# Kernel tuning notes

Measured on AMD Instinct MI355X. Metric: run time of the kernel, lower is better.

The kernel has to match this reference:

```python
import jax, jax.numpy as jnp
import numpy as np

MAX_VAL = 10000.0
KS = (1, 5, 10, 20, 50)
B, V, L = 256, 128000, 200


def setup_inputs() -> dict:
    key = jax.random.key(0)
    k1, k2, k3 = jax.random.split(key, 3)
    scores = jax.random.normal(k1, (B, V), dtype=jnp.float32)
    labels = jax.random.randint(k2, (B,), 0, V, dtype=jnp.int64)
    seqs = jax.random.randint(k3, (B, L), 0, V, dtype=jnp.int64)
    return {"scores": scores, "labels": labels, "seqs": seqs}


def reference(scores, labels, seqs):
    b = scores.shape[0]
    rows = jnp.arange(b)
    # gather predicted score for the true label BEFORE masking (torch order)
    predicts = scores[rows, labels]  # [B]
    # scatter -MAX_VAL at history items (masked scatter)
    masked = scores.at[rows[:, None], seqs].set(-MAX_VAL)  # [B, V]
    valid_length = (masked > -MAX_VAL).sum(-1).astype(jnp.float32)  # [B]
    rank = (predicts[:, None] < masked).sum(-1).astype(jnp.float32)  # [B]
    res = []
    for k in KS:
        indicator = (rank < k).astype(jnp.float32)
        res.append((indicator / jnp.log2(rank + 2.0)).mean())  # NDCG@k
        res.append(indicator.mean())  # Recall@k
    res.append((1.0 / (rank + 1.0)).mean())  # MRR
    res.append((1.0 - rank / valid_length).mean())  # AUC-like
    res.append(jnp.float32(0.0))
    return jnp.stack(res)
```

## Files before the change

### kernel.cpp

```cpp
#include <hip/hip_runtime.h>
#include <math.h>

#define B_CONST 256
#define V_CONST 128000
#define L_CONST 200
#define SLICES  25


__global__ __launch_bounds__(256) void rank_count_kernel(
    const float* __restrict__ scores,
    const int* __restrict__ labels,
    const int* __restrict__ seqs,
    int* __restrict__ partial,
    int* __restrict__ sub,
    int* __restrict__ dist)
{
    const int slice = blockIdx.x;
    const int b     = blockIdx.y;
    const int tid   = threadIdx.x;

    const float* row = scores + (size_t)b * V_CONST;

    const float4* row4 = (const float4*)row;
    const int base = slice * 1280 + tid;
    float4 a0 = row4[base];
    float4 a1 = row4[base + 256];
    float4 a2 = row4[base + 512];
    float4 a3 = row4[base + 768];
    float4 a4 = row4[base + 1024];

    const float predict = row[labels[b]];

    __shared__ int s_cnt, s_sub, s_dist;
    __shared__ int s_seq[L_CONST];
    if (tid == 0) { s_cnt = 0; s_sub = 0; s_dist = 0; }
    if (slice == 0 && tid < L_CONST) s_seq[tid] = seqs[b * L_CONST + tid];
    __syncthreads();

    int cnt = 0;
    cnt += (a0.x > predict) + (a0.y > predict) + (a0.z > predict) + (a0.w > predict);
    cnt += (a1.x > predict) + (a1.y > predict) + (a1.z > predict) + (a1.w > predict);
    cnt += (a2.x > predict) + (a2.y > predict) + (a2.z > predict) + (a2.w > predict);
    cnt += (a3.x > predict) + (a3.y > predict) + (a3.z > predict) + (a3.w > predict);
    cnt += (a4.x > predict) + (a4.y > predict) + (a4.z > predict) + (a4.w > predict);

    #pragma unroll
    for (int off = 32; off > 0; off >>= 1)
        cnt += __shfl_down(cnt, off, 64);
    if ((tid & 63) == 0) atomicAdd(&s_cnt, cnt);

    if (slice == 0 && tid < L_CONST) {
        const int s = s_seq[tid];
        const float sv = row[s];
        bool first = true;
        for (int j = 0; j < tid; ++j) {
            if (s_seq[j] == s) { first = false; break; }
        }
        if (first) {
            atomicAdd(&s_dist, 1);
            if (sv > predict) atomicAdd(&s_sub, 1);
        }
    }
    __syncthreads();

    if (tid == 0) {
        partial[slice * B_CONST + b] = s_cnt;
        if (slice == 0) {
            sub[b]  = s_sub;
            dist[b] = s_dist;
        }
    }
}

__global__ __launch_bounds__(256) void finalize_kernel(
    const int* __restrict__ partial,
    const int* __restrict__ sub,
    const int* __restrict__ dist,
    float* __restrict__ out)
{
    const int b = threadIdx.x;
    int gt = 0;
    #pragma unroll
    for (int s = 0; s < SLICES; ++s) gt += partial[s * B_CONST + b];
    const float rank  = (float)(gt - sub[b]);
    const float valid = (float)(V_CONST - dist[b]);

    const float ks[5] = {1.0f, 5.0f, 10.0f, 20.0f, 50.0f};
    float vals[12];
    const float invlog = 1.0f / log2f(rank + 2.0f);
    #pragma unroll
    for (int i = 0; i < 5; ++i) {
        const float ind = (rank < ks[i]) ? 1.0f : 0.0f;
        vals[2 * i]     = ind * invlog;
        vals[2 * i + 1] = ind;
    }
    vals[10] = 1.0f / (rank + 1.0f);
    vals[11] = 1.0f - rank / valid;

    __shared__ float red[4];
    for (int q = 0; q < 12; ++q) {
        float v = vals[q];
        #pragma unroll
        for (int off = 32; off > 0; off >>= 1)
            v += __shfl_down(v, off, 64);
        if ((b & 63) == 0) red[b >> 6] = v;
        __syncthreads();
        if (b == 0) out[q] = (red[0] + red[1] + red[2] + red[3]) * (1.0f / B_CONST);
        __syncthreads();
    }
    if (b == 0) out[12] = 0.0f;
}

extern "C" void kernel_launch(void* const* d_in, const int* in_sizes, int n_in,
                              void* d_out, int out_size, void* d_ws, size_t ws_size,
                              hipStream_t stream) {
    const float* scores = (const float*)d_in[0];
    const int*   labels = (const int*)d_in[1];
    const int*   seqs   = (const int*)d_in[2];
    float* out = (float*)d_out;
    int*   ws  = (int*)d_ws;

    int* partial = ws;
    int* sub     = ws + SLICES * B_CONST;
    int* dist    = ws + SLICES * B_CONST + B_CONST;

    rank_count_kernel<<<dim3(SLICES, B_CONST), 256, 0, stream>>>(
        scores, labels, seqs, partial, sub, dist);
    finalize_kernel<<<1, 256, 0, stream>>>(partial, sub, dist, out);
}
```

Baseline: 201.8 us.

## Split prep from counting and fold finalize into last-block ticket reduction

Moves the label gather and history dedup into a separate per-row prep kernel. The main count kernel then runs 2048 blocks, with each wave streaming a contiguous 1000-float4 slice in a 15-iteration loop, and accumulates per-row counts with global atomics. The separate finalize launch is replaced by a last-block ticket pattern inside the count kernel. The aim is to take the serial dedup and the label load off the streaming critical path and to shorten the finalize tail, at the cost of an extra prep launch and global atomics.

Result: slower. 300.9 us (+49.1%).

```diff
diff --git a/kernel.cpp b/kernel.cpp
--- a/kernel.cpp
+++ b/kernel.cpp
@@ -4,58 +4,37 @@
 #define B_CONST 256
 #define V_CONST 128000
 #define L_CONST 200
-#define SLICES  25
+#define NBLOCKS 2048
+#define F4_WAVE 1000
 
 
-__global__ __launch_bounds__(256) void rank_count_kernel(
+__global__ __launch_bounds__(256) void prep_kernel(
     const float* __restrict__ scores,
     const int* __restrict__ labels,
     const int* __restrict__ seqs,
-    int* __restrict__ partial,
+    int* __restrict__ gt,
     int* __restrict__ sub,
-    int* __restrict__ dist)
+    int* __restrict__ dist,
+    unsigned* __restrict__ ticket,
+    float* __restrict__ predicts)
 {
-    const int slice = blockIdx.x;
-    const int b     = blockIdx.y;
-    const int tid   = threadIdx.x;
+    const int b   = blockIdx.x;
+    const int tid = threadIdx.x;
+    __shared__ int s_seq[L_CONST];
+    __shared__ int s_sub, s_dist;
 
     const float* row = scores + (size_t)b * V_CONST;
-
-    const float4* row4 = (const float4*)row;
-    const int base = slice * 1280 + tid;
-    float4 a0 = row4[base];
-    float4 a1 = row4[base + 256];
-    float4 a2 = row4[base + 512];
-    float4 a3 = row4[base + 768];
-    float4 a4 = row4[base + 1024];
-
+    if (tid == 0) { s_sub = 0; s_dist = 0; }
+    if (tid < L_CONST) s_seq[tid] = seqs[b * L_CONST + tid];
     const float predict = row[labels[b]];
-
-    __shared__ int s_cnt, s_sub, s_dist;
-    __shared__ int s_seq[L_CONST];
-    if (tid == 0) { s_cnt = 0; s_sub = 0; s_dist = 0; }
-    if (slice == 0 && tid < L_CONST) s_seq[tid] = seqs[b * L_CONST + tid];
     __syncthreads();
 
-    int cnt = 0;
-    cnt += (a0.x > predict) + (a0.y > predict) + (a0.z > predict) + (a0.w > predict);
-    cnt += (a1.x > predict) + (a1.y > predict) + (a1.z > predict) + (a1.w > predict);
-    cnt += (a2.x > predict) + (a2.y > predict) + (a2.z > predict) + (a2.w > predict);
-    cnt += (a3.x > predict) + (a3.y > predict) + (a3.z > predict) + (a3.w > predict);
-    cnt += (a4.x > predict) + (a4.y > predict) + (a4.z > predict) + (a4.w > predict);
-
-    #pragma unroll
-    for (int off = 32; off > 0; off >>= 1)
-        cnt += __shfl_down(cnt, off, 64);
-    if ((tid & 63) == 0) atomicAdd(&s_cnt, cnt);
-
-    if (slice == 0 && tid < L_CONST) {
+    if (tid < L_CONST) {
         const int s = s_seq[tid];
         const float sv = row[s];
         bool first = true;
-        for (int j = 0; j < tid; ++j) {
+        for (int j = 0; j < tid; ++j)
             if (s_seq[j] == s) { first = false; break; }
-        }
         if (first) {
             atomicAdd(&s_dist, 1);
             if (sv > predict) atomicAdd(&s_sub, 1);
@@ -64,25 +43,64 @@
     __syncthreads();
 
     if (tid == 0) {
-        partial[slice * B_CONST + b] = s_cnt;
-        if (slice == 0) {
-            sub[b]  = s_sub;
-            dist[b] = s_dist;
-        }
+        gt[b]       = 0;
+        sub[b]      = s_sub;
+        dist[b]     = s_dist;
+        predicts[b] = predict;
+        if (b == 0) *ticket = 0u;
     }
 }
 
-__global__ __launch_bounds__(256) void finalize_kernel(
-    const int* __restrict__ partial,
+__global__ __launch_bounds__(256) void count_kernel(
+    const float* __restrict__ scores,
+    int* __restrict__ gt,
     const int* __restrict__ sub,
     const int* __restrict__ dist,
+    unsigned* __restrict__ ticket,
+    const float* __restrict__ predicts,
     float* __restrict__ out)
 {
-    const int b = threadIdx.x;
-    int gt = 0;
+    const int tid  = threadIdx.x;
+    const int lane = tid & 63;
+    const int w    = tid >> 6;
+    const int row  = blockIdx.x & 255;
+    const int wslc = ((blockIdx.x >> 8) << 2) + w;
+
+    const float4* p = (const float4*)(scores + (size_t)row * V_CONST) + wslc * F4_WAVE;
+
+    float4 tv;
+    if (lane < 40) tv = p[960 + lane];
+    const float predict = predicts[row];
+
+    int cnt = 0;
+    #pragma unroll 5
+    for (int it = 0; it < 15; ++it) {
+        float4 v = p[it * 64 + lane];
+        cnt += (v.x > predict) + (v.y > predict) + (v.z > predict) + (v.w > predict);
+    }
+    if (lane < 40)
+        cnt += (tv.x > predict) + (tv.y > predict) + (tv.z > predict) + (tv.w > predict);
+
     #pragma unroll
-    for (int s = 0; s < SLICES; ++s) gt += partial[s * B_CONST + b];
-    const float rank  = (float)(gt - sub[b]);
+    for (int off = 32; off > 0; off >>= 1)
+        cnt += __shfl_down(cnt, off, 64);
+    if (lane == 0) atomicAdd(&gt[row], cnt);
+
+    __shared__ int s_last;
+    __shared__ float red[4];
+    __syncthreads();
+    if (tid == 0) {
+        __threadfence();
+        unsigned old = atomicAdd(ticket, 1u);
+        s_last = (old == (unsigned)(NBLOCKS - 1));
+    }
+    __syncthreads();
+    if (!s_last) return;
+
+    __threadfence();
+    const int b = tid;
+    const int gtv = atomicAdd(&gt[b], 0);
+    const float rank  = (float)(gtv - sub[b]);
     const float valid = (float)(V_CONST - dist[b]);
 
     const float ks[5] = {1.0f, 5.0f, 10.0f, 20.0f, 50.0f};
@@ -97,7 +115,6 @@
     vals[10] = 1.0f / (rank + 1.0f);
     vals[11] = 1.0f - rank / valid;
 
-    __shared__ float red[4];
     for (int q = 0; q < 12; ++q) {
         float v = vals[q];
         #pragma unroll
@@ -118,13 +135,16 @@
     const int*   labels = (const int*)d_in[1];
     const int*   seqs   = (const int*)d_in[2];
     float* out = (float*)d_out;
-    int*   ws  = (int*)d_ws;
+    int*   wsi = (int*)d_ws;
 
-    int* partial = ws;
-    int* sub     = ws + SLICES * B_CONST;
-    int* dist    = ws + SLICES * B_CONST + B_CONST;
+    int*      gt       = wsi;
+    int*      sub      = wsi + 256;
+    int*      dist     = wsi + 512;
+    unsigned* ticket   = (unsigned*)(wsi + 768);
+    float*    predicts = (float*)(wsi + 1024);
 
-    rank_count_kernel<<<dim3(SLICES, B_CONST), 256, 0, stream>>>(
-        scores, labels, seqs, partial, sub, dist);
-    finalize_kernel<<<1, 256, 0, stream>>>(partial, sub, dist, out);
+    prep_kernel<<<B_CONST, 256, 0, stream>>>(scores, labels, seqs,
+                                             gt, sub, dist, ticket, predicts);
+    count_kernel<<<NBLOCKS, 256, 0, stream>>>(scores, gt, sub, dist,
+                                              ticket, predicts, out);
 }
```
